# Performance work log

Measured on AMD Instinct MI355X. Metric: run time of the kernel, lower is better.

The kernel has to match this reference:

```python
import jax, jax.numpy as jnp
import numpy as np

DIM = 1024
NUM_HEADS = 16
HEAD_DIM = DIM // NUM_HEADS
SCALE = HEAD_DIM ** -0.5


def setup_inputs() -> dict:
    key = jax.random.key(0)
    k_x, k_qkv, k_pw, k_pb = jax.random.split(key, 4)
    B, N, C = 1, 4096, 3 * DIM
    x = jax.random.normal(k_x, (B, N, C), dtype=jnp.float32)
    # torch nn.Linear stores weight as [out, in]; y = x @ W.T + b
    W_qkv = jax.random.normal(k_qkv, (3 * DIM, 3 * DIM), dtype=jnp.float32) * (3 * DIM) ** -0.5
    W_proj = jax.random.normal(k_pw, (DIM, DIM), dtype=jnp.float32) * DIM ** -0.5
    b_proj = jax.random.normal(k_pb, (DIM,), dtype=jnp.float32) * 0.01
    return {"x": x, "W_qkv": W_qkv, "W_proj": W_proj, "b_proj": b_proj}


def reference(x, W_qkv, W_proj, b_proj):
    B, N, C = x.shape  # C == 3*DIM
    qkv = x @ W_qkv.T  # [B, N, 3*DIM]
    qkv = qkv.reshape(B, N, 3, NUM_HEADS, HEAD_DIM).transpose(2, 0, 3, 1, 4)
    q, k, v = qkv[0], qkv[1], qkv[2]  # each [B, H, N, hd]
    attn = jnp.einsum('bhnd,bhmd->bhnm', q, k) * SCALE
    attn = jax.nn.softmax(attn, axis=-1)
    out = jnp.einsum('bhnm,bhmd->bhnd', attn, v)  # [B, H, N, hd]
    out = out.transpose(0, 2, 1, 3).reshape(B, N, DIM)
    return out @ W_proj.T + b_proj
```

## Files before the change

### kernel.cpp

```cpp
#include <hip/hip_runtime.h>
#include <hip/hip_fp16.h>

#define SEQ     4096
#define NHEADS  16
#define HDIM    64
#define DIMSZ   1024
#define ATT_SCALE 0.125f

static constexpr size_t QSZ = (size_t)NHEADS * SEQ * HDIM;

typedef __attribute__((ext_vector_type(8))) short short8;
typedef __attribute__((ext_vector_type(4))) short s16x4;
typedef __attribute__((ext_vector_type(8))) unsigned short ushort8;
typedef __attribute__((ext_vector_type(4))) float f32x4;
#define MFMA_F16(a, b, c) __builtin_amdgcn_mfma_f32_16x16x32_f16((a), (b), (c), 0, 0, 0)

__device__ __forceinline__ unsigned short f2hu(float x) {
    __half h = __float2half(x);
    return *reinterpret_cast<unsigned short*>(&h);
}
__device__ __forceinline__ float hu2f(unsigned short u) {
    __half h = *reinterpret_cast<__half*>(&u);
    return __half2float(h);
}
__device__ __forceinline__ void split8h(float4 f0, float4 f1, ushort8& h, ushort8& l) {
    const float v[8] = {f0.x, f0.y, f0.z, f0.w, f1.x, f1.y, f1.z, f1.w};
    #pragma unroll
    for (int i = 0; i < 8; ++i) {
        const unsigned short hi = f2hu(v[i]);
        h[i] = hi;
        l[i] = f2hu(v[i] - hu2f(hi));
    }
}

typedef __attribute__((address_space(1))) const unsigned int g_u32;
typedef __attribute__((address_space(3))) unsigned int lds_u32;
__device__ __forceinline__ void async16(unsigned short* lds, const unsigned short* g) {
    __builtin_amdgcn_global_load_lds((g_u32*)g, (lds_u32*)lds, 16, 0, 0);
}

__global__ void prep_split(const float* __restrict__ x, unsigned short* __restrict__ xh,
                           unsigned short* __restrict__ xl, int nx,
                           const float* __restrict__ w0, unsigned short* __restrict__ w0h,
                           int n0,
                           const float* __restrict__ w1, unsigned short* __restrict__ w1h,
                           int n1)
{
    const int stride = gridDim.x * blockDim.x;
    const int tid = blockIdx.x * blockDim.x + threadIdx.x;
    for (int i = tid; i < (nx >> 2); i += stride) {
        float4 v = ((const float4*)x)[i];
        ushort4 h, l;
        h.x = f2hu(v.x); l.x = f2hu(v.x - hu2f(h.x));
        h.y = f2hu(v.y); l.y = f2hu(v.y - hu2f(h.y));
        h.z = f2hu(v.z); l.z = f2hu(v.z - hu2f(h.z));
        h.w = f2hu(v.w); l.w = f2hu(v.w - hu2f(h.w));
        ((ushort4*)xh)[i] = h; ((ushort4*)xl)[i] = l;
    }
    for (int i = tid; i < (n0 >> 2); i += stride) {
        float4 v = ((const float4*)w0)[i];
        ushort4 h;
        h.x = f2hu(v.x); h.y = f2hu(v.y); h.z = f2hu(v.z); h.w = f2hu(v.w);
        ((ushort4*)w0h)[i] = h;
    }
    for (int i = tid; i < (n1 >> 2); i += stride) {
        float4 v = ((const float4*)w1)[i];
        ushort4 h;
        h.x = f2hu(v.x); h.y = f2hu(v.y); h.z = f2hu(v.z); h.w = f2hu(v.w);
        ((ushort4*)w1h)[i] = h;
    }
}

__global__ __launch_bounds__(512, 2)
void qkv_gemm_8ph(const unsigned short* __restrict__ AHg,
                  const unsigned short* __restrict__ ALg,
                  const unsigned short* __restrict__ BHg,
                  unsigned short* __restrict__ QH, unsigned short* __restrict__ QL,
                  unsigned short* __restrict__ KH, unsigned short* __restrict__ VT)
{
    constexpr int K3 = 3072;
    constexpr int NT = K3 / 32;
    __shared__ __align__(16) unsigned short ring[3 * 24576];

    const int t  = threadIdx.x;
    const int wv = t >> 6;
    const int ln = t & 63;
    const int lx = ln & 15;
    const int q4 = ln >> 4;
    const int wr = wv >> 2;
    const int wc = wv & 3;

    const int bid = blockIdx.x;
    const int swz = (bid & 7) * 24 + (bid >> 3);
    const int m0 = (swz / 12) * 256;
    const int n0 = (swz % 12) * 256;

    const int srow = t >> 2;
    const int sg8  = (((t & 3) ^ ((t >> 3) & 3)) << 3);

    auto stage3a = [&](int tt, int b) {
        const int kk = tt << 5;
        unsigned short* Lb = &ring[b * 24576 + wv * 512];
        const size_t ga = (size_t)(m0 + srow) * K3 + kk + sg8;
        async16(Lb,               AHg + ga);
        async16(Lb + 4096,        AHg + ga + (size_t)128 * K3);
        async16(Lb + 8192,        ALg + ga);
    };
    auto stage3b = [&](int tt, int b) {
        const int kk = tt << 5;
        unsigned short* Lb = &ring[b * 24576 + wv * 512];
        const size_t ga = (size_t)(m0 + srow) * K3 + kk + sg8;
        const size_t gb = (size_t)(n0 + srow) * K3 + kk + sg8;
        async16(Lb + 12288,       ALg + ga + (size_t)128 * K3);
        async16(Lb + 16384,       BHg + gb);
        async16(Lb + 20480,       BHg + gb + (size_t)128 * K3);
    };

    f32x4 acc[8][4];
    #pragma unroll
    for (int mf = 0; mf < 8; ++mf)
        #pragma unroll
        for (int nf = 0; nf < 4; ++nf)
            acc[mf][nf] = (f32x4){0.f, 0.f, 0.f, 0.f};

    stage3a(0, 0); stage3b(0, 0);
    stage3a(1, 1); stage3b(1, 1);
    asm volatile("s_waitcnt vmcnt(6)" ::: "memory");
    __builtin_amdgcn_s_barrier();

    const int aswz8 = ((q4 ^ ((lx >> 1) & 3)) << 3);
    const int arow0 = (wr * 128 + lx) * 32 + aswz8;
    const int brow0 = (wc * 64  + lx) * 32 + aswz8;

    int c = 0;
    for (int kt = 0; kt < NT; ++kt) {
        const unsigned short* AHp = &ring[c * 24576];
        const unsigned short* ALp = AHp + 8192;
        const unsigned short* Bp  = AHp + 16384;
        int c2 = c + 2; if (c2 >= 3) c2 -= 3;
        const bool pf = (kt + 2 < NT);

        short8 bfr[4];
        #pragma unroll
        for (int ph = 0; ph < 4; ++ph) {
            if (ph == 0) {
                #pragma unroll
                for (int nf = 0; nf < 4; ++nf)
                    bfr[nf] = *(const short8*)&Bp[brow0 + nf * 512];
            }
            short8 ahf[2], alf[2];
            #pragma unroll
            for (int i = 0; i < 2; ++i) {
                const int mo = arow0 + (ph * 2 + i) * 512;
                ahf[i] = *(const short8*)&AHp[mo];
                alf[i] = *(const short8*)&ALp[mo];
            }
            if (ph == 0 && pf) stage3a(kt + 2, c2);
            if (ph == 1 && pf) stage3b(kt + 2, c2);
            __builtin_amdgcn_s_barrier();
            __builtin_amdgcn_s_setprio(1);
            #pragma unroll
            for (int nf = 0; nf < 4; ++nf)
                #pragma unroll
                for (int i = 0; i < 2; ++i) {
                    acc[ph * 2 + i][nf] = MFMA_F16(ahf[i], bfr[nf], acc[ph * 2 + i][nf]);
                    acc[ph * 2 + i][nf] = MFMA_F16(alf[i], bfr[nf], acc[ph * 2 + i][nf]);
                }
            __builtin_amdgcn_s_setprio(0);
            if (ph == 3) {
                if (pf) asm volatile("s_waitcnt vmcnt(6)" ::: "memory");
                else    asm volatile("s_waitcnt vmcnt(0)" ::: "memory");
            }
            __builtin_amdgcn_s_barrier();
        }
        ++c; if (c == 3) c = 0;
    }

    const int part = n0 >> 10;
    #pragma unroll
    for (int nf = 0; nf < 4; ++nf) {
        const int colb = n0 + wc * 64 + nf * 16;
        const int head = (colb >> 6) & 15;
        const int d0   = (colb & 63) + lx;
        if (part == 0) {
            #pragma unroll
            for (int mf = 0; mf < 8; ++mf) {
                const int row0 = m0 + wr * 128 + mf * 16 + q4 * 4;
                #pragma unroll
                for (int r = 0; r < 4; ++r) {
                    const float v = acc[mf][nf][r] * ATT_SCALE;
                    const unsigned short h = f2hu(v);
                    const size_t idx = ((size_t)head * SEQ + row0 + r) * HDIM + d0;
                    QH[idx] = h;
                    QL[idx] = f2hu(v - hu2f(h));
                }
            }
        } else if (part == 1) {
            #pragma unroll
            for (int mf = 0; mf < 8; ++mf) {
                const int row0 = m0 + wr * 128 + mf * 16 + q4 * 4;
                #pragma unroll
                for (int r = 0; r < 4; ++r) {
                    const size_t idx = ((size_t)head * SEQ + row0 + r) * HDIM + d0;
                    KH[idx] = f2hu(acc[mf][nf][r]);
                }
            }
        } else {
            unsigned short* base = VT + ((size_t)head * HDIM + d0) * SEQ;
            #pragma unroll
            for (int mf = 0; mf < 8; ++mf) {
                const int row0 = m0 + wr * 128 + mf * 16 + q4 * 4;
                ushort4 o;
                o.x = f2hu(acc[mf][nf][0]); o.y = f2hu(acc[mf][nf][1]);
                o.z = f2hu(acc[mf][nf][2]); o.w = f2hu(acc[mf][nf][3]);
                *(ushort4*)(base + row0) = o;
            }
        }
    }
}

template <int MODE, bool ASPLIT>
__global__ __launch_bounds__(256, 3)
void mfma_gemm_abt(const float* __restrict__ A,
                   const unsigned short* __restrict__ AHg,
                   const unsigned short* __restrict__ ALg,
                   const unsigned short* __restrict__ BHg,
                   const float* __restrict__ bias, float* __restrict__ C,
                   unsigned short* __restrict__ QH, unsigned short* __restrict__ QL,
                   unsigned short* __restrict__ KH, unsigned short* __restrict__ VT,
                   int M, int N, int K)
{
    constexpr int LDP = ASPLIT ? 32 : 40;
    __shared__ unsigned short AHs[128 * LDP];
    __shared__ unsigned short ALs[128 * LDP];
    __shared__ unsigned short BHs[128 * LDP];

    const int t  = threadIdx.x;
    const int wv = t >> 6;
    const int ln = t & 63;
    const int lx = ln & 15;
    const int q4 = ln >> 4;
    const int m0 = blockIdx.y * 128;
    const int n0 = blockIdx.x * 128;

    f32x4 acc[2][8];
    #pragma unroll
    for (int mf = 0; mf < 2; ++mf)
        #pragma unroll
        for (int nf = 0; nf < 8; ++nf)
            acc[mf][nf] = (f32x4){0.f, 0.f, 0.f, 0.f};

    for (int k0 = 0; k0 < K; k0 += 32) {
        if constexpr (ASPLIT) {
            const int rowc = ln >> 2;
            const int c8   = (ln & 3) << 3;
            #pragma unroll
            for (int rep = 0; rep < 2; ++rep) {
                const int chunk = rep * 4 + wv;
                const int r = chunk * 16 + rowc;
                const size_t goff = (size_t)(m0 + r) * K + k0 + c8;
                const size_t boff = (size_t)(n0 + r) * K + k0 + c8;
                async16(&AHs[chunk * 16 * LDP], AHg + goff);
                async16(&ALs[chunk * 16 * LDP], ALg + goff);
                async16(&BHs[chunk * 16 * LDP], BHg + boff);
            }
        } else {
            #pragma unroll
            for (int rep = 0; rep < 2; ++rep) {
                const int task = rep * 256 + t;
                const int r  = task >> 2;
                const int sg = (task & 3) << 3;
                {
                    const float* p = A + (size_t)(m0 + r) * K + k0 + sg;
                    float4 f0 = *(const float4*)p;
                    float4 f1 = *(const float4*)(p + 4);
                    ushort8 h, l; split8h(f0, f1, h, l);
                    *(ushort8*)&AHs[r * LDP + sg] = h;
                    *(ushort8*)&ALs[r * LDP + sg] = l;
                }
                {
                    const size_t off = (size_t)(n0 + r) * K + k0 + sg;
                    *(ushort8*)&BHs[r * LDP + sg] = *(const ushort8*)(BHg + off);
                }
            }
        }
        __syncthreads();

        short8 ah[2], al[2];
        #pragma unroll
        for (int mf = 0; mf < 2; ++mf) {
            const int row = wv * 32 + mf * 16 + lx;
            ah[mf] = *(const short8*)&AHs[row * LDP + q4 * 8];
            al[mf] = *(const short8*)&ALs[row * LDP + q4 * 8];
        }
        #pragma unroll
        for (int nf = 0; nf < 8; ++nf) {
            const short8 bh = *(const short8*)&BHs[(nf * 16 + lx) * LDP + q4 * 8];
            #pragma unroll
            for (int mf = 0; mf < 2; ++mf) {
                acc[mf][nf] = MFMA_F16(ah[mf], bh, acc[mf][nf]);
                acc[mf][nf] = MFMA_F16(al[mf], bh, acc[mf][nf]);
            }
        }
        __syncthreads();
    }

    if constexpr (MODE == 0) {
        #pragma unroll
        for (int nf = 0; nf < 8; ++nf) {
            const int col = n0 + nf * 16 + lx;
            const float bv = bias[col];
            #pragma unroll
            for (int mf = 0; mf < 2; ++mf) {
                const int row0 = m0 + wv * 32 + mf * 16 + q4 * 4;
                #pragma unroll
                for (int r = 0; r < 4; ++r)
                    C[(size_t)(row0 + r) * N + col] = acc[mf][nf][r] + bv;
            }
        }
    } else {
        const int part = n0 >> 10;
        #pragma unroll
        for (int nf = 0; nf < 8; ++nf) {
            const int colb = n0 + nf * 16;
            const int head = (colb >> 6) & 15;
            const int d0   = (colb & 63) + lx;
            if (part == 0) {
                #pragma unroll
                for (int mf = 0; mf < 2; ++mf) {
                    const int row0 = m0 + wv * 32 + mf * 16 + q4 * 4;
                    #pragma unroll
                    for (int r = 0; r < 4; ++r) {
                        const float v = acc[mf][nf][r] * ATT_SCALE;
                        const unsigned short h = f2hu(v);
                        const size_t idx = ((size_t)head * SEQ + row0 + r) * HDIM + d0;
                        QH[idx] = h;
                        QL[idx] = f2hu(v - hu2f(h));
                    }
                }
            } else if (part == 1) {
                #pragma unroll
                for (int mf = 0; mf < 2; ++mf) {
                    const int row0 = m0 + wv * 32 + mf * 16 + q4 * 4;
                    #pragma unroll
                    for (int r = 0; r < 4; ++r) {
                        const size_t idx = ((size_t)head * SEQ + row0 + r) * HDIM + d0;
                        KH[idx] = f2hu(acc[mf][nf][r]);
                    }
                }
            } else {
                unsigned short* base = VT + ((size_t)head * HDIM + d0) * SEQ;
                #pragma unroll
                for (int mf = 0; mf < 2; ++mf) {
                    const int row0 = m0 + wv * 32 + mf * 16 + q4 * 4;
                    ushort4 o;
                    o.x = f2hu(acc[mf][nf][0]); o.y = f2hu(acc[mf][nf][1]);
                    o.z = f2hu(acc[mf][nf][2]); o.w = f2hu(acc[mf][nf][3]);
                    *(ushort4*)(base + row0) = o;
                }
            }
        }
    }
}

__global__ __launch_bounds__(256, 2)
void attn_mfma(const unsigned short* __restrict__ QHg,
               const unsigned short* __restrict__ QLg,
               const unsigned short* __restrict__ KHg,
               const unsigned short* __restrict__ VTg,
               unsigned short* __restrict__ AttnH,
               unsigned short* __restrict__ AttnL)
{
    __shared__ __align__(16) char shraw[35840];
    unsigned short* KHI = (unsigned short*)shraw;
    unsigned short* VS  = (unsigned short*)(shraw + 17408);
    float* obuf = (float*)shraw;
    float* lbuf = (float*)(shraw + 34816);

    const int t  = threadIdx.x;
    const int wv = t >> 6;
    const int ln = t & 63;
    const int q4 = ln >> 4;
    const int lx = ln & 15;
    const int qb   = blockIdx.x;
    const int head = blockIdx.y;

    const unsigned short* Kh = KHg + (size_t)head * SEQ * HDIM;
    const unsigned short* Vg = VTg + (size_t)head * HDIM * SEQ;

    short8 qh[4][2], ql[4][2];
    #pragma unroll
    for (int qt = 0; qt < 4; ++qt)
        #pragma unroll
        for (int s = 0; s < 2; ++s) {
            const size_t off = ((size_t)head * SEQ + (size_t)qb * 64 + qt * 16 + lx) * HDIM
                             + s * 32 + q4 * 8;
            qh[qt][s] = *(const short8*)(QHg + off);
            ql[qt][s] = *(const short8*)(QLg + off);
        }

    f32x4 o_acc[4][4];
    float l_part[4] = {0.f, 0.f, 0.f, 0.f};
    #pragma unroll
    for (int dt = 0; dt < 4; ++dt)
        #pragma unroll
        for (int qt = 0; qt < 4; ++qt)
            o_acc[dt][qt] = (f32x4){0.f, 0.f, 0.f, 0.f};

    ushort8 bk[4], bv[4];
    auto load_tile = [&](int kbase) {
        #pragma unroll
        for (int it = 0; it < 4; ++it) {
            const int idx = it * 256 + t;
            const int r  = idx >> 3, c8 = (idx & 7) << 3;
            bk[it] = *(const ushort8*)(Kh + (size_t)(kbase + r) * HDIM + c8);
            const int rv = idx >> 4, cv = (idx & 15) << 3;
            bv[it] = *(const ushort8*)(Vg + (size_t)rv * SEQ + kbase + cv);
        }
    };

    load_tile(0);
    for (int mt = 0; mt < SEQ / 128; ++mt) {
        #pragma unroll
        for (int it = 0; it < 4; ++it) {
            const int idx = it * 256 + t;
            const int r  = idx >> 3, c8 = (idx & 7) << 3;
            *(ushort8*)&KHI[r * 68 + c8] = bk[it];
            const int rv = idx >> 4, cv = (idx & 15) << 3;
            *(ushort8*)&VS[rv * 136 + cv] = bv[it];
        }
        __syncthreads();

        if (mt + 1 < SEQ / 128) load_tile((mt + 1) * 128);

        short8 phi[4];
        #pragma unroll
        for (int st = 0; st < 2; ++st) {
            const int kr = st * 64 + wv * 16 + lx;
            short8 kfh[2];
            #pragma unroll
            for (int s = 0; s < 2; ++s)
                kfh[s] = *(const short8*)&KHI[kr * 68 + s * 32 + q4 * 8];
            #pragma unroll
            for (int qt = 0; qt < 4; ++qt) {
                f32x4 sa = (f32x4){0.f, 0.f, 0.f, 0.f};
                __builtin_amdgcn_s_setprio(1);
                #pragma unroll
                for (int s = 0; s < 2; ++s) {
                    sa = MFMA_F16(kfh[s], qh[qt][s], sa);
                    sa = MFMA_F16(kfh[s], ql[qt][s], sa);
                }
                __builtin_amdgcn_s_setprio(0);
                #pragma unroll
                for (int r = 0; r < 4; ++r) {
                    const float e = __expf(sa[r]);
                    l_part[qt] += e;
                    phi[qt][st * 4 + r] = (short)f2hu(e);
                }
            }
        }

        #pragma unroll
        for (int dt = 0; dt < 4; ++dt) {
            const int vrow = (dt * 16 + lx) * 136 + wv * 16 + q4 * 4;
            const s16x4 v0 = *(const s16x4*)&VS[vrow];
            const s16x4 v1 = *(const s16x4*)&VS[vrow + 64];
            short8 vf;
            #pragma unroll
            for (int i = 0; i < 4; ++i) { vf[i] = v0[i]; vf[i + 4] = v1[i]; }
            __builtin_amdgcn_s_setprio(1);
            #pragma unroll
            for (int qt = 0; qt < 4; ++qt)
                o_acc[dt][qt] = MFMA_F16(vf, phi[qt], o_acc[dt][qt]);
            __builtin_amdgcn_s_setprio(0);
        }
        __syncthreads();
    }

    float lw[4];
    #pragma unroll
    for (int qt = 0; qt < 4; ++qt) {
        float l = l_part[qt];
        l += __shfl_xor(l, 16);
        l += __shfl_xor(l, 32);
        lw[qt] = l;
    }
    if (q4 == 0) {
        #pragma unroll
        for (int qt = 0; qt < 4; ++qt)
            lbuf[wv * 64 + qt * 16 + lx] = lw[qt];
    }
    #pragma unroll
    for (int p = 0; p < 2; ++p) {
        #pragma unroll
        for (int dd = 0; dd < 2; ++dd) {
            const int dt = p * 2 + dd;
            #pragma unroll
            for (int qt = 0; qt < 4; ++qt)
                #pragma unroll
                for (int r = 0; r < 4; ++r)
                    obuf[wv * 2176 + (dd * 16 + q4 * 4 + r) * 68 + qt * 16 + lx]
                        = o_acc[dt][qt][r];
        }
        __syncthreads();
        {
            const int q  = t >> 2;
            const int dg = (t & 3) << 3;
            const float linv = 1.f / (lbuf[q] + lbuf[64 + q] + lbuf[128 + q] + lbuf[192 + q]);
            ushort8 ho, lo;
            #pragma unroll
            for (int j = 0; j < 8; ++j) {
                const int dloc = dg + j;
                const float s = obuf[dloc * 68 + q] + obuf[2176 + dloc * 68 + q]
                              + obuf[4352 + dloc * 68 + q] + obuf[6528 + dloc * 68 + q];
                const float v = s * linv;
                const unsigned short h = f2hu(v);
                ho[j] = (short)h;
                lo[j] = (short)f2hu(v - hu2f(h));
            }
            const size_t ob = (size_t)(qb * 64 + q) * DIMSZ + head * HDIM + p * 32 + dg;
            *(ushort8*)(AttnH + ob) = ho;
            *(ushort8*)(AttnL + ob) = lo;
        }
        __syncthreads();
    }
}

extern "C" void kernel_launch(void* const* d_in, const int* in_sizes, int n_in,
                              void* d_out, int out_size, void* d_ws,
                              size_t ws_size, hipStream_t stream)
{
    const float* x     = (const float*)d_in[0];
    const float* Wqkv  = (const float*)d_in[1];
    const float* Wproj = (const float*)d_in[2];
    const float* bproj = (const float*)d_in[3];
    float* out = (float*)d_out;

    const size_t NWQ = (size_t)3072 * 3072;
    const size_t NWP = (size_t)1024 * 1024;
    const size_t NX  = (size_t)4096 * 3072;

    unsigned short* ub = (unsigned short*)d_ws;
    unsigned short* AttnH = ub;
    unsigned short* AttnL = ub + QSZ;
    unsigned short* QHg = ub + 2 * QSZ;
    unsigned short* QLg = ub + 3 * QSZ;
    unsigned short* KHg = ub + 4 * QSZ;
    unsigned short* VTg = ub + 5 * QSZ;
    unsigned short* WQH = ub + 6 * QSZ;
    unsigned short* WPH = WQH + NWQ;
    unsigned short* XH  = WPH + NWP;
    unsigned short* XL  = XH + NX;
    const bool xsplit = ws_size >= 121634816ull;

    prep_split<<<2048, 256, 0, stream>>>(
        xsplit ? x : nullptr, XH, XL, xsplit ? (int)NX : 0,
        Wqkv, WQH, (int)NWQ, Wproj, WPH, (int)NWP);

    if (xsplit) {
        qkv_gemm_8ph<<<192, 512, 0, stream>>>(
            XH, XL, WQH, QHg, QLg, KHg, VTg);
    } else {
        dim3 g1(3 * DIMSZ / 128, SEQ / 128);
        mfma_gemm_abt<1, false><<<g1, 256, 0, stream>>>(
            x, nullptr, nullptr, WQH, nullptr, nullptr,
            QHg, QLg, KHg, VTg, SEQ, 3 * DIMSZ, 3 * DIMSZ);
    }

    dim3 g2(SEQ / 64, NHEADS);
    attn_mfma<<<g2, 256, 0, stream>>>(QHg, QLg, KHg, VTg, AttnH, AttnL);

    dim3 g3(DIMSZ / 128, SEQ / 128);
    mfma_gemm_abt<0, true><<<g3, 256, 0, stream>>>(
        nullptr, AttnH, AttnL, WPH, bproj, out,
        nullptr, nullptr, nullptr, nullptr, SEQ, DIMSZ, DIMSZ);
}
```

Baseline: 473.4 us.

## Double-buffer K/V shared-memory tiles in attention kernel to halve barriers

```diff
diff --git a/kernel.cpp b/kernel.cpp
--- a/kernel.cpp
+++ b/kernel.cpp
@@ -371,11 +371,13 @@
                unsigned short* __restrict__ AttnH,
                unsigned short* __restrict__ AttnL)
 {
-    __shared__ __align__(16) char shraw[35840];
-    unsigned short* KHI = (unsigned short*)shraw;
-    unsigned short* VS  = (unsigned short*)(shraw + 17408);
+    __shared__ __align__(16) char shraw[70656];
+    unsigned short* KHI_A = (unsigned short*)shraw;
+    unsigned short* VS_A  = (unsigned short*)(shraw + 17408);
+    unsigned short* KHI_B = (unsigned short*)(shraw + 34816);
+    unsigned short* VS_B  = (unsigned short*)(shraw + 52224);
     float* obuf = (float*)shraw;
-    float* lbuf = (float*)(shraw + 34816);
+    float* lbuf = (float*)(shraw + 69632);
 
     const int t  = threadIdx.x;
     const int wv = t >> 6;
@@ -418,21 +420,17 @@
             bv[it] = *(const ushort8*)(Vg + (size_t)rv * SEQ + kbase + cv);
         }
     };
-
-    load_tile(0);
-    for (int mt = 0; mt < SEQ / 128; ++mt) {
+    auto write_tile = [&](unsigned short* KHIc, unsigned short* VSc) {
         #pragma unroll
         for (int it = 0; it < 4; ++it) {
             const int idx = it * 256 + t;
             const int r  = idx >> 3, c8 = (idx & 7) << 3;
-            *(ushort8*)&KHI[r * 68 + c8] = bk[it];
+            *(ushort8*)&KHIc[r * 68 + c8] = bk[it];
             const int rv = idx >> 4, cv = (idx & 15) << 3;
-            *(ushort8*)&VS[rv * 136 + cv] = bv[it];
-        }
-        __syncthreads();
-
-        if (mt + 1 < SEQ / 128) load_tile((mt + 1) * 128);
-
+            *(ushort8*)&VSc[rv * 136 + cv] = bv[it];
+        }
+    };
+    auto compute_tile = [&](const unsigned short* KHIc, const unsigned short* VSc) {
         short8 phi[4];
         #pragma unroll
         for (int st = 0; st < 2; ++st) {
@@ -440,7 +438,7 @@
             short8 kfh[2];
             #pragma unroll
             for (int s = 0; s < 2; ++s)
-                kfh[s] = *(const short8*)&KHI[kr * 68 + s * 32 + q4 * 8];
+                kfh[s] = *(const short8*)&KHIc[kr * 68 + s * 32 + q4 * 8];
             #pragma unroll
             for (int qt = 0; qt < 4; ++qt) {
                 f32x4 sa = (f32x4){0.f, 0.f, 0.f, 0.f};
@@ -459,12 +457,11 @@
                 }
             }
         }
-
         #pragma unroll
         for (int dt = 0; dt < 4; ++dt) {
             const int vrow = (dt * 16 + lx) * 136 + wv * 16 + q4 * 4;
-            const s16x4 v0 = *(const s16x4*)&VS[vrow];
-            const s16x4 v1 = *(const s16x4*)&VS[vrow + 64];
+            const s16x4 v0 = *(const s16x4*)&VSc[vrow];
+            const s16x4 v1 = *(const s16x4*)&VSc[vrow + 64];
             short8 vf;
             #pragma unroll
             for (int i = 0; i < 4; ++i) { vf[i] = v0[i]; vf[i + 4] = v1[i]; }
@@ -473,6 +470,25 @@
             for (int qt = 0; qt < 4; ++qt)
                 o_acc[dt][qt] = MFMA_F16(vf, phi[qt], o_acc[dt][qt]);
             __builtin_amdgcn_s_setprio(0);
+        }
+    };
+
+    load_tile(0);
+    write_tile(KHI_A, VS_A);
+    __syncthreads();
+
+    for (int i = 0; i < SEQ / 256; ++i) {
+        const int mt = 2 * i;
+        load_tile((mt + 1) * 128);
+        compute_tile(KHI_A, VS_A);
+        write_tile(KHI_B, VS_B);
+        __syncthreads();
+        if (mt + 2 < SEQ / 128) {
+            load_tile((mt + 2) * 128);
+            compute_tile(KHI_B, VS_B);
+            write_tile(KHI_A, VS_A);
+        } else {
+            compute_tile(KHI_B, VS_B);
         }
         __syncthreads();
     }
```

Measured after the change: 508.8 us. 1.07x slower.

## Double-buffer K/V tiles with async global-to-LDS copies and XOR swizzle

Applied to the files above, without the earlier changes.

```diff
diff --git a/kernel.cpp b/kernel.cpp
--- a/kernel.cpp
+++ b/kernel.cpp
@@ -371,9 +371,11 @@
                unsigned short* __restrict__ AttnH,
                unsigned short* __restrict__ AttnL)
 {
-    __shared__ __align__(16) char shraw[35840];
-    unsigned short* KHI = (unsigned short*)shraw;
-    unsigned short* VS  = (unsigned short*)(shraw + 17408);
+    __shared__ __align__(16) char shraw[65536];
+    unsigned short* KA = (unsigned short*)shraw;
+    unsigned short* VA = (unsigned short*)(shraw + 16384);
+    unsigned short* KB = (unsigned short*)(shraw + 32768);
+    unsigned short* VB = (unsigned short*)(shraw + 49152);
     float* obuf = (float*)shraw;
     float* lbuf = (float*)(shraw + 34816);
 
@@ -407,32 +409,22 @@
         for (int qt = 0; qt < 4; ++qt)
             o_acc[dt][qt] = (f32x4){0.f, 0.f, 0.f, 0.f};
 
-    ushort8 bk[4], bv[4];
-    auto load_tile = [&](int kbase) {
-        #pragma unroll
-        for (int it = 0; it < 4; ++it) {
-            const int idx = it * 256 + t;
-            const int r  = idx >> 3, c8 = (idx & 7) << 3;
-            bk[it] = *(const ushort8*)(Kh + (size_t)(kbase + r) * HDIM + c8);
-            const int rv = idx >> 4, cv = (idx & 15) << 3;
-            bv[it] = *(const ushort8*)(Vg + (size_t)rv * SEQ + kbase + cv);
+    const int rK8 = t >> 3;
+    const int gck = ((t & 7) ^ (rK8 & 7)) << 3;
+    const int rV4 = t >> 4;
+    const int gcv = ((t & 15) ^ (rV4 & 7)) << 3;
+
+    auto issue_tile = [&](int kbase, unsigned short* KX, unsigned short* VX) {
+        #pragma unroll
+        for (int c = 0; c < 4; ++c) {
+            async16(KX + (c * 32 + wv * 8) * 64,
+                    Kh + (size_t)(kbase + c * 32 + rK8) * HDIM + gck);
+            async16(VX + (c * 16 + wv * 4) * 128,
+                    Vg + (size_t)(c * 16 + rV4) * SEQ + kbase + gcv);
         }
     };
 
-    load_tile(0);
-    for (int mt = 0; mt < SEQ / 128; ++mt) {
-        #pragma unroll
-        for (int it = 0; it < 4; ++it) {
-            const int idx = it * 256 + t;
-            const int r  = idx >> 3, c8 = (idx & 7) << 3;
-            *(ushort8*)&KHI[r * 68 + c8] = bk[it];
-            const int rv = idx >> 4, cv = (idx & 15) << 3;
-            *(ushort8*)&VS[rv * 136 + cv] = bv[it];
-        }
-        __syncthreads();
-
-        if (mt + 1 < SEQ / 128) load_tile((mt + 1) * 128);
-
+    auto compute_tile = [&](const unsigned short* KX, const unsigned short* VX) {
         short8 phi[4];
         #pragma unroll
         for (int st = 0; st < 2; ++st) {
@@ -440,7 +432,7 @@
             short8 kfh[2];
             #pragma unroll
             for (int s = 0; s < 2; ++s)
-                kfh[s] = *(const short8*)&KHI[kr * 68 + s * 32 + q4 * 8];
+                kfh[s] = *(const short8*)&KX[kr * 64 + (((s * 4 + q4) ^ (kr & 7)) << 3)];
             #pragma unroll
             for (int qt = 0; qt < 4; ++qt) {
                 f32x4 sa = (f32x4){0.f, 0.f, 0.f, 0.f};
@@ -459,12 +451,14 @@
                 }
             }
         }
-
+        const int colb = wv * 32 + q4 * 8;
+        const int sl0  = colb >> 4;
+        const int sub  = (colb & 15) >> 1;
         #pragma unroll
         for (int dt = 0; dt < 4; ++dt) {
-            const int vrow = (dt * 16 + lx) * 136 + wv * 16 + q4 * 4;
-            const s16x4 v0 = *(const s16x4*)&VS[vrow];
-            const s16x4 v1 = *(const s16x4*)&VS[vrow + 64];
+            const int vr = dt * 16 + lx;
+            const s16x4 v0 = *(const s16x4*)&VX[vr * 128 + (((sl0    ) ^ (vr & 7)) << 3) + sub];
+            const s16x4 v1 = *(const s16x4*)&VX[vr * 128 + (((sl0 + 8) ^ (vr & 7)) << 3) + sub];
             short8 vf;
             #pragma unroll
             for (int i = 0; i < 4; ++i) { vf[i] = v0[i]; vf[i + 4] = v1[i]; }
@@ -474,6 +468,18 @@
                 o_acc[dt][qt] = MFMA_F16(vf, phi[qt], o_acc[dt][qt]);
             __builtin_amdgcn_s_setprio(0);
         }
+    };
+
+    issue_tile(0, KA, VA);
+    __syncthreads();
+
+    for (int i = 0; i < SEQ / 256; ++i) {
+        const int mt = 2 * i;
+        if (mt + 1 < SEQ / 128) issue_tile((mt + 1) * 128, KB, VB);
+        compute_tile(KA, VA);
+        __syncthreads();
+        if (mt + 2 < SEQ / 128) issue_tile((mt + 2) * 128, KA, VA);
+        compute_tile(KB, VB);
         __syncthreads();
     }
 
```

After: 427.0 us. 9.8% less time.
